# Kernel optimization log

Hardware: AMD Instinct MI355X
Metric: run time of the kernel (lower is better)

Reference implementation:

```python
import jax, jax.numpy as jnp
import numpy as np

B, S, D = 4, 2048, 1024
H = 16
HD = D // H


def setup_inputs() -> dict:
    key = jax.random.key(0)
    ks = jax.random.split(key, 5)
    scale = 0.02
    return {
        "x": jax.random.normal(ks[0], (B, S, D), dtype=jnp.float32),
        "wq": jax.random.normal(ks[1], (D, D), dtype=jnp.float32) * scale,
        "wk": jax.random.normal(ks[2], (D, D), dtype=jnp.float32) * scale,
        "wv": jax.random.normal(ks[3], (D, D), dtype=jnp.float32) * scale,
        "wo": jax.random.normal(ks[4], (D, D), dtype=jnp.float32) * scale,
    }


def reference(x, wq, wk, wv, wo):
    b, s, _ = x.shape
    # project and split heads: [b, h, s, hd]
    def proj(w):
        return jnp.einsum('bsd,de->bse', x, w).reshape(b, s, H, HD).transpose(0, 2, 1, 3)
    q, k, v = proj(wq), proj(wk), proj(wv)
    scores = jnp.einsum('bhqd,bhkd->bhqk', q, k)
    causal = jnp.tril(jnp.ones((s, s), dtype=bool))  # True = keep
    scores = jnp.where(causal, scores, -jnp.inf)
    attn = jax.nn.softmax(scores / jnp.sqrt(jnp.float32(HD)), axis=-1)
    ctx = jnp.einsum('bhqk,bhkd->bhqd', attn, v)
    ctx = ctx.transpose(0, 2, 1, 3).reshape(b, s, D)
    return jnp.einsum('bsd,de->bse', ctx, wo)
```

## Files before the change

kernel.cpp:

```cpp
#include <hip/hip_runtime.h>

#define S_LEN 2048
#define D_DIM 1024
#define NH    16
#define HD    64
#define BATCH 4
#define M_ROWS 8192

typedef __attribute__((ext_vector_type(8))) short bf16x8;
typedef __attribute__((ext_vector_type(4))) float f32x4;
typedef __attribute__((ext_vector_type(8))) unsigned short u16x8;

__device__ __forceinline__ unsigned short f2bf(float f) {
    unsigned u = __builtin_bit_cast(unsigned, f);
    u = (u + 0x7fffu + ((u >> 16) & 1u)) >> 16;
    return (unsigned short)u;
}
__device__ __forceinline__ unsigned pack2(float a, float b) {
    unsigned ua = __builtin_bit_cast(unsigned, a);
    unsigned ub = __builtin_bit_cast(unsigned, b);
    return ((ua + 0x8000u) >> 16) | ((ub + 0x8000u) & 0xffff0000u);
}

__device__ __forceinline__ void gload16(const void* g, void* l) {
    __builtin_amdgcn_global_load_lds((const __attribute__((address_space(1))) unsigned*)g,
                                     (__attribute__((address_space(3))) unsigned*)l,
                                     16, 0, 0);
}

__global__ __launch_bounds__(256) void castx_k(const float* __restrict__ x,
                                               unsigned short* __restrict__ o) {
    size_t i = (size_t)blockIdx.x * 256 + threadIdx.x;
    const float4* xf = (const float4*)x;
    float4 a = xf[2 * i], b = xf[2 * i + 1];
    u16x8 v;
    v[0] = f2bf(a.x); v[1] = f2bf(a.y); v[2] = f2bf(a.z); v[3] = f2bf(a.w);
    v[4] = f2bf(b.x); v[5] = f2bf(b.y); v[6] = f2bf(b.z); v[7] = f2bf(b.w);
    *(u16x8*)(o + i * 8) = v;
}

__global__ __launch_bounds__(256) void wprep_k(const float* __restrict__ w0, const float* __restrict__ w1,
                                               const float* __restrict__ w2, const float* __restrict__ w3,
                                               unsigned short* __restrict__ o0, unsigned short* __restrict__ o1,
                                               unsigned short* __restrict__ o2, unsigned short* __restrict__ o3) {
    __shared__ float sT[64][65];
    const float* w; unsigned short* o;
    switch (blockIdx.z) {
        case 0: w = w0; o = o0; break;
        case 1: w = w1; o = o1; break;
        case 2: w = w2; o = o2; break;
        default: w = w3; o = o3; break;
    }
    const float sc = (blockIdx.z == 0) ? 0.18033688011112042f : 1.0f;
    const int t = threadIdx.x;
    const int k0 = blockIdx.y * 64, n0 = blockIdx.x * 64;
    const int r = t >> 4, cq = t & 15;
#pragma unroll
    for (int it = 0; it < 4; ++it) {
        int k = r + it * 16;
        float4 v = *(const float4*)&w[(size_t)(k0 + k) * D_DIM + n0 + cq * 4];
        sT[k][cq * 4 + 0] = v.x; sT[k][cq * 4 + 1] = v.y;
        sT[k][cq * 4 + 2] = v.z; sT[k][cq * 4 + 3] = v.w;
    }
    __syncthreads();
    const int n = t >> 2, ch = t & 3;
    union { unsigned short s[8]; uint4 v; } p0, p1;
#pragma unroll
    for (int j = 0; j < 8; ++j) p0.s[j] = f2bf(sT[ch * 16 + j][n] * sc);
#pragma unroll
    for (int j = 0; j < 8; ++j) p1.s[j] = f2bf(sT[ch * 16 + 8 + j][n] * sc);
    *(uint4*)&o[(size_t)(n0 + n) * D_DIM + k0 + ch * 16]     = p0.v;
    *(uint4*)&o[(size_t)(n0 + n) * D_DIM + k0 + ch * 16 + 8] = p1.v;
}

__device__ __forceinline__ void gemm_core(const unsigned short* __restrict__ A,
                                          const unsigned short* __restrict__ Bt,
                                          unsigned short* sA, unsigned short* sB,
                                          int m0, int n0, int t, f32x4 acc[4][4])
{
    const int lane = t & 63, w = t >> 6;
    const int mm = lane & 15, quad = lane >> 4;
    const int wm = w >> 1, wn = w & 1;

    auto stage = [&](int k0, int bufi) {
#pragma unroll
        for (int it = 0; it < 2; ++it) {
            int idx = t + it * 256;
            int m = idx >> 2, j = idx & 3;
            int g = (j - (m >> 1)) & 3;
            gload16(A  + ((size_t)(m0 + m) * D_DIM + k0 + g * 8), (void*)&sA[bufi * 4096 + idx * 8]);
            gload16(Bt + ((size_t)(n0 + m) * D_DIM + k0 + g * 8), (void*)&sB[bufi * 4096 + idx * 8]);
        }
    };

    stage(0, 0);
    for (int kt = 0; kt < D_DIM / 32; ++kt) {
        const int bufo = (kt & 1) * 4096;
        __syncthreads();
        if (kt + 1 < D_DIM / 32) stage((kt + 1) * 32, 1 - (kt & 1));

        bf16x8 af[4], bfr[4];
#pragma unroll
        for (int mi = 0; mi < 4; ++mi) {
            int m = wm * 64 + mi * 16 + mm;
            int slot = (quad + (m >> 1)) & 3;
            af[mi] = *(const bf16x8*)&sA[bufo + m * 32 + slot * 8];
        }
#pragma unroll
        for (int ni = 0; ni < 4; ++ni) {
            int n = wn * 64 + ni * 16 + mm;
            int slot = (quad + (n >> 1)) & 3;
            bfr[ni] = *(const bf16x8*)&sB[bufo + n * 32 + slot * 8];
        }
#pragma unroll
        for (int mi = 0; mi < 4; ++mi)
#pragma unroll
            for (int ni = 0; ni < 4; ++ni)
                acc[mi][ni] = __builtin_amdgcn_mfma_f32_16x16x32_bf16(af[mi], bfr[ni], acc[mi][ni], 0, 0, 0);
    }
}

__global__ __launch_bounds__(256) void gemmqkv_k(const unsigned short* __restrict__ A,
                                                 const unsigned short* __restrict__ Bt,
                                                 unsigned short* __restrict__ qb,
                                                 unsigned short* __restrict__ kb,
                                                 unsigned short* __restrict__ vt)
{
    __shared__ unsigned short sA[2 * 128 * 32];
    __shared__ unsigned short sB[2 * 128 * 32];
    const int t = threadIdx.x;
    const int lane = t & 63, w = t >> 6;
    const int mm = lane & 15, quad = lane >> 4;
    const int wm = w >> 1, wn = w & 1;
    const int m0 = blockIdx.y * 128, n0 = blockIdx.x * 128;

    f32x4 acc[4][4];
#pragma unroll
    for (int i = 0; i < 4; ++i)
#pragma unroll
        for (int j = 0; j < 4; ++j) acc[i][j] = (f32x4){0.f, 0.f, 0.f, 0.f};

    gemm_core(A, Bt, sA, sB, m0, n0, t, acc);

    const int widx = n0 >> 10;
    if (widx == 2) {
#pragma unroll
        for (int mi = 0; mi < 4; ++mi) {
            int rglob = m0 + wm * 64 + mi * 16 + quad * 4;
            int bb = rglob >> 11, ss = rglob & (S_LEN - 1);
#pragma unroll
            for (int ni = 0; ni < 4; ++ni) {
                int c = (n0 & 1023) + wn * 64 + ni * 16 + mm;
                int h = c >> 6, hd = c & 63;
                union { unsigned short s[4]; unsigned long long ll; } pk;
#pragma unroll
                for (int r = 0; r < 4; ++r) pk.s[r] = f2bf(acc[mi][ni][r]);
                *(unsigned long long*)&vt[((size_t)(bb * NH + h) * HD + hd) * S_LEN + ss] = pk.ll;
            }
        }
    } else {
        unsigned short* outp = widx ? kb : qb;
        const int nl0 = n0 & 1023;
#pragma unroll
        for (int mi = 0; mi < 4; ++mi)
#pragma unroll
            for (int ni = 0; ni < 4; ++ni)
#pragma unroll
                for (int r = 0; r < 4; ++r)
                    outp[(size_t)(m0 + wm * 64 + mi * 16 + quad * 4 + r) * D_DIM +
                         nl0 + wn * 64 + ni * 16 + mm] = f2bf(acc[mi][ni][r]);
    }
}

__global__ __launch_bounds__(256) void gemmo_k(const unsigned short* __restrict__ A,
                                               const unsigned short* __restrict__ Bt,
                                               float* __restrict__ C)
{
    __shared__ unsigned short sA[2 * 128 * 32];
    __shared__ unsigned short sB[2 * 128 * 32];
    const int t = threadIdx.x;
    const int lane = t & 63, w = t >> 6;
    const int mm = lane & 15, quad = lane >> 4;
    const int wm = w >> 1, wn = w & 1;
    const int m0 = blockIdx.y * 128, n0 = blockIdx.x * 128;

    f32x4 acc[4][4];
#pragma unroll
    for (int i = 0; i < 4; ++i)
#pragma unroll
        for (int j = 0; j < 4; ++j) acc[i][j] = (f32x4){0.f, 0.f, 0.f, 0.f};

    gemm_core(A, Bt, sA, sB, m0, n0, t, acc);

#pragma unroll
    for (int mi = 0; mi < 4; ++mi)
#pragma unroll
        for (int ni = 0; ni < 4; ++ni)
#pragma unroll
            for (int r = 0; r < 4; ++r)
                C[(size_t)(m0 + wm * 64 + mi * 16 + quad * 4 + r) * D_DIM +
                  n0 + wn * 64 + ni * 16 + mm] = acc[mi][ni][r];
}

__global__ __launch_bounds__(512, 4) void attn_k(const unsigned short* __restrict__ Q,
                                                 const unsigned short* __restrict__ K,
                                                 const unsigned short* __restrict__ Vt,
                                                 unsigned short* __restrict__ ctx)
{
    __shared__ unsigned short sK [2][128 * 64];
    __shared__ unsigned short sVT[2][64 * 128];
    __shared__ unsigned short sP [128 * 64];
    const int t = threadIdx.x;
    const int lane = t & 63, w = t >> 6;
    const int mm = lane & 15, quad = lane >> 4;
    const int pair = blockIdx.x, bh = blockIdx.y;
    const int b = bh >> 4, hh = bh & 15;
    const size_t rowbase = (size_t)b * S_LEN;
    const int coff = hh * HD;
    const unsigned short* Vh = Vt + (size_t)bh * HD * S_LEN;

    auto stage = [&](int kt, int bufi) {
#pragma unroll
        for (int it = 0; it < 2; ++it) {
            int idx = t + it * 512;
            int key = idx >> 3, jk = idx & 7, gk = jk ^ (key & 7);
            gload16(K + (rowbase + kt * 128 + key) * D_DIM + coff + gk * 8,
                    (void*)&sK[bufi][idx * 8]);
            int hd = idx >> 4, jv = idx & 15, gv = jv ^ (hd & 15);
            gload16(Vh + (size_t)hd * S_LEN + kt * 128 + gv * 8,
                    (void*)&sVT[bufi][idx * 8]);
        }
    };

    u16x8 onesu;
#pragma unroll
    for (int j = 0; j < 8; ++j) onesu[j] = 0x3F80;
    const bf16x8 ones = __builtin_bit_cast(bf16x8, onesu);

    for (int sidx = 0; sidx < 2; ++sidx) {
        const int qt = sidx ? (15 - pair) : pair;
        const int q0 = qt * 128;

        bf16x8 qf[2];
#pragma unroll
        for (int kk = 0; kk < 2; ++kk)
            qf[kk] = *(const bf16x8*)(Q + (rowbase + q0 + w * 16 + mm) * D_DIM
                                        + coff + kk * 32 + quad * 8);
        f32x4 o[4], lacc;
        lacc = (f32x4){0.f, 0.f, 0.f, 0.f};
#pragma unroll
        for (int hf = 0; hf < 4; ++hf) o[hf] = (f32x4){0.f, 0.f, 0.f, 0.f};

        const int nkt = qt + 1;
        const int qr = q0 + w * 16 + mm;
        const int qrmax = q0 + w * 16 + 15;
        const int m = w * 16 + mm;

        stage(0, 0);
        for (int kt = 0; kt < nkt; ++kt) {
            const int buf = kt & 1;
            __syncthreads();
            if (kt + 1 < nkt) stage(kt + 1, 1 - buf);

#pragma unroll
            for (int kh = 0; kh < 2; ++kh) {
                const int k0 = kt * 128 + kh * 64;
                if (k0 > qrmax) continue;

                f32x4 sacc[4];
#pragma unroll
                for (int kf = 0; kf < 4; ++kf) sacc[kf] = (f32x4){0.f, 0.f, 0.f, 0.f};
#pragma unroll
                for (int kk = 0; kk < 2; ++kk) {
                    bf16x8 ak[4];
#pragma unroll
                    for (int kf = 0; kf < 4; ++kf) {
                        int key = kh * 64 + kf * 16 + mm;
                        int slot = (kk * 4 + quad) ^ (key & 7);
                        ak[kf] = *(const bf16x8*)&sK[buf][key * 64 + slot * 8];
                    }
#pragma unroll
                    for (int kf = 0; kf < 4; ++kf)
                        sacc[kf] = __builtin_amdgcn_mfma_f32_16x16x32_bf16(ak[kf], qf[kk], sacc[kf], 0, 0, 0);
                }

                const bool needmask = (k0 + 63) > (q0 + w * 16);
#pragma unroll
                for (int kf = 0; kf < 4; ++kf) {
                    float p[4];
#pragma unroll
                    for (int r = 0; r < 4; ++r) {
                        p[r] = __builtin_amdgcn_exp2f(sacc[kf][r]);
                        if (needmask && (k0 + kf * 16 + quad * 4 + r) > qr) p[r] = 0.f;
                    }
                    unsigned lo = pack2(p[0], p[1]), hi = pack2(p[2], p[3]);
                    int slot = (kf * 2 + (quad >> 1)) ^ (m & 7);
                    *(unsigned long long*)&sP[m * 64 + slot * 8 + (quad & 1) * 4] =
                        ((unsigned long long)hi << 32) | lo;
                }

#pragma unroll
                for (int kk = 0; kk < 2; ++kk) {
                    bf16x8 pf, vf[4];
                    {
                        int slot = (kk * 4 + quad) ^ (m & 7);
                        pf = *(const bf16x8*)&sP[m * 64 + slot * 8];
                    }
#pragma unroll
                    for (int hf = 0; hf < 4; ++hf) {
                        int hd = hf * 16 + mm;
                        int c = kh * 8 + kk * 4 + quad;
                        int slot = c ^ (hd & 15);
                        vf[hf] = *(const bf16x8*)&sVT[buf][hd * 128 + slot * 8];
                    }
                    lacc = __builtin_amdgcn_mfma_f32_16x16x32_bf16(pf, ones, lacc, 0, 0, 0);
#pragma unroll
                    for (int hf = 0; hf < 4; ++hf)
                        o[hf] = __builtin_amdgcn_mfma_f32_16x16x32_bf16(pf, vf[hf], o[hf], 0, 0, 0);
                }
            }
        }
        __syncthreads();

#pragma unroll
        for (int r = 0; r < 4; ++r) {
            float inv = 1.f / lacc[r];
            int row = q0 + w * 16 + quad * 4 + r;
#pragma unroll
            for (int hf = 0; hf < 4; ++hf)
                ctx[(rowbase + row) * D_DIM + coff + hf * 16 + mm] = f2bf(o[hf][r] * inv);
        }
    }
}

extern "C" void kernel_launch(void* const* d_in, const int* in_sizes, int n_in,
                              void* d_out, int out_size, void* d_ws, size_t ws_size,
                              hipStream_t stream)
{
    const float* x  = (const float*)d_in[0];
    const float* wq = (const float*)d_in[1];
    const float* wk = (const float*)d_in[2];
    const float* wv = (const float*)d_in[3];
    const float* wo = (const float*)d_in[4];

    const size_t XE = (size_t)M_ROWS * D_DIM;
    const size_t WE = (size_t)D_DIM * D_DIM;
    unsigned short* ws  = (unsigned short*)d_ws;
    unsigned short* xbf = ws;
    unsigned short* wt0 = xbf + XE;
    unsigned short* wt1 = wt0 + WE;
    unsigned short* wt2 = wt1 + WE;
    unsigned short* wt3 = wt2 + WE;
    unsigned short* qb  = wt3 + WE;
    unsigned short* kb  = qb + XE;
    unsigned short* vt  = kb + XE;
    unsigned short* cb  = vt + XE;

    castx_k<<<dim3(M_ROWS * D_DIM / (256 * 8)), 256, 0, stream>>>(x, xbf);
    wprep_k<<<dim3(16, 16, 4), 256, 0, stream>>>(wq, wk, wv, wo, wt0, wt1, wt2, wt3);

    gemmqkv_k<<<dim3(3 * D_DIM / 128, M_ROWS / 128), 256, 0, stream>>>(xbf, wt0, qb, kb, vt);

    attn_k<<<dim3(8, BATCH * NH), 512, 0, stream>>>(qb, kb, vt, cb);

    gemmo_k<<<dim3(D_DIM / 128, M_ROWS / 128), 256, 0, stream>>>(cb, wt3, (float*)d_out);
}
```

Before: 280.2 us.

## Single-buffer GEMM staging and shrink attention key tiles to 64

The GEMM core drops double-buffered LDS staging for a single buffer, loading and then synchronizing before each k-step. This halves GEMM shared memory but stops overlapping loads with MFMA work. The attention kernel moves from 128-key to 64-key tiles with a matching swizzle, halving its LDS footprint and masking less work per tile, at the cost of twice as many iterations and barriers.

```diff
diff --git a/kernel.cpp b/kernel.cpp
--- a/kernel.cpp
+++ b/kernel.cpp
@@ -82,35 +82,30 @@
     const int mm = lane & 15, quad = lane >> 4;
     const int wm = w >> 1, wn = w & 1;
 
-    auto stage = [&](int k0, int bufi) {
+    for (int k0 = 0; k0 < D_DIM; k0 += 32) {
+        __syncthreads();
 #pragma unroll
         for (int it = 0; it < 2; ++it) {
             int idx = t + it * 256;
             int m = idx >> 2, j = idx & 3;
             int g = (j - (m >> 1)) & 3;
-            gload16(A  + ((size_t)(m0 + m) * D_DIM + k0 + g * 8), (void*)&sA[bufi * 4096 + idx * 8]);
-            gload16(Bt + ((size_t)(n0 + m) * D_DIM + k0 + g * 8), (void*)&sB[bufi * 4096 + idx * 8]);
-        }
-    };
-
-    stage(0, 0);
-    for (int kt = 0; kt < D_DIM / 32; ++kt) {
-        const int bufo = (kt & 1) * 4096;
+            gload16(A  + ((size_t)(m0 + m) * D_DIM + k0 + g * 8), (void*)&sA[idx * 8]);
+            gload16(Bt + ((size_t)(n0 + m) * D_DIM + k0 + g * 8), (void*)&sB[idx * 8]);
+        }
         __syncthreads();
-        if (kt + 1 < D_DIM / 32) stage((kt + 1) * 32, 1 - (kt & 1));
 
         bf16x8 af[4], bfr[4];
 #pragma unroll
         for (int mi = 0; mi < 4; ++mi) {
             int m = wm * 64 + mi * 16 + mm;
             int slot = (quad + (m >> 1)) & 3;
-            af[mi] = *(const bf16x8*)&sA[bufo + m * 32 + slot * 8];
+            af[mi] = *(const bf16x8*)&sA[m * 32 + slot * 8];
         }
 #pragma unroll
         for (int ni = 0; ni < 4; ++ni) {
             int n = wn * 64 + ni * 16 + mm;
             int slot = (quad + (n >> 1)) & 3;
-            bfr[ni] = *(const bf16x8*)&sB[bufo + n * 32 + slot * 8];
+            bfr[ni] = *(const bf16x8*)&sB[n * 32 + slot * 8];
         }
 #pragma unroll
         for (int mi = 0; mi < 4; ++mi)
@@ -126,8 +121,8 @@
                                                  unsigned short* __restrict__ kb,
                                                  unsigned short* __restrict__ vt)
 {
-    __shared__ unsigned short sA[2 * 128 * 32];
-    __shared__ unsigned short sB[2 * 128 * 32];
+    __shared__ unsigned short sA[128 * 32];
+    __shared__ unsigned short sB[128 * 32];
     const int t = threadIdx.x;
     const int lane = t & 63, w = t >> 6;
     const int mm = lane & 15, quad = lane >> 4;
@@ -176,8 +171,8 @@
                                                const unsigned short* __restrict__ Bt,
                                                float* __restrict__ C)
 {
-    __shared__ unsigned short sA[2 * 128 * 32];
-    __shared__ unsigned short sB[2 * 128 * 32];
+    __shared__ unsigned short sA[128 * 32];
+    __shared__ unsigned short sB[128 * 32];
     const int t = threadIdx.x;
     const int lane = t & 63, w = t >> 6;
     const int mm = lane & 15, quad = lane >> 4;
@@ -207,8 +202,8 @@
                                                  const unsigned short* __restrict__ Vt,
                                                  unsigned short* __restrict__ ctx)
 {
-    __shared__ unsigned short sK [2][128 * 64];
-    __shared__ unsigned short sVT[2][64 * 128];
+    __shared__ unsigned short sK [2][64 * 64];
+    __shared__ unsigned short sVT[2][64 * 64];
     __shared__ unsigned short sP [128 * 64];
     const int t = threadIdx.x;
     const int lane = t & 63, w = t >> 6;
@@ -219,18 +214,8 @@
     const int coff = hh * HD;
     const unsigned short* Vh = Vt + (size_t)bh * HD * S_LEN;
 
-    auto stage = [&](int kt, int bufi) {
-#pragma unroll
-        for (int it = 0; it < 2; ++it) {
-            int idx = t + it * 512;
-            int key = idx >> 3, jk = idx & 7, gk = jk ^ (key & 7);
-            gload16(K + (rowbase + kt * 128 + key) * D_DIM + coff + gk * 8,
-                    (void*)&sK[bufi][idx * 8]);
-            int hd = idx >> 4, jv = idx & 15, gv = jv ^ (hd & 15);
-            gload16(Vh + (size_t)hd * S_LEN + kt * 128 + gv * 8,
-                    (void*)&sVT[bufi][idx * 8]);
-        }
-    };
+    const int sc_ = t >> 3, sj = t & 7;
+    const int sgk = sj ^ (sc_ & 7);
 
     u16x8 onesu;
 #pragma unroll
@@ -251,73 +236,76 @@
 #pragma unroll
         for (int hf = 0; hf < 4; ++hf) o[hf] = (f32x4){0.f, 0.f, 0.f, 0.f};
 
-        const int nkt = qt + 1;
+        const int nkt = 2 * qt + 2;
         const int qr = q0 + w * 16 + mm;
         const int qrmax = q0 + w * 16 + 15;
         const int m = w * 16 + mm;
 
-        stage(0, 0);
+        gload16(K  + (rowbase + sc_) * D_DIM + coff + sgk * 8, (void*)&sK[0][t * 8]);
+        gload16(Vh + (size_t)sc_ * S_LEN + sgk * 8,            (void*)&sVT[0][t * 8]);
+
         for (int kt = 0; kt < nkt; ++kt) {
             const int buf = kt & 1;
             __syncthreads();
-            if (kt + 1 < nkt) stage(kt + 1, 1 - buf);
-
-#pragma unroll
-            for (int kh = 0; kh < 2; ++kh) {
-                const int k0 = kt * 128 + kh * 64;
-                if (k0 > qrmax) continue;
-
-                f32x4 sacc[4];
-#pragma unroll
-                for (int kf = 0; kf < 4; ++kf) sacc[kf] = (f32x4){0.f, 0.f, 0.f, 0.f};
-#pragma unroll
-                for (int kk = 0; kk < 2; ++kk) {
-                    bf16x8 ak[4];
-#pragma unroll
-                    for (int kf = 0; kf < 4; ++kf) {
-                        int key = kh * 64 + kf * 16 + mm;
-                        int slot = (kk * 4 + quad) ^ (key & 7);
-                        ak[kf] = *(const bf16x8*)&sK[buf][key * 64 + slot * 8];
-                    }
-#pragma unroll
-                    for (int kf = 0; kf < 4; ++kf)
-                        sacc[kf] = __builtin_amdgcn_mfma_f32_16x16x32_bf16(ak[kf], qf[kk], sacc[kf], 0, 0, 0);
+            if (kt + 1 < nkt) {
+                const int k1 = (kt + 1) * 64;
+                gload16(K  + (rowbase + k1 + sc_) * D_DIM + coff + sgk * 8,
+                        (void*)&sK[1 - buf][t * 8]);
+                gload16(Vh + (size_t)sc_ * S_LEN + k1 + sgk * 8,
+                        (void*)&sVT[1 - buf][t * 8]);
+            }
+            const int k0 = kt * 64;
+            if (k0 > qrmax) continue;
+
+            f32x4 sacc[4];
+#pragma unroll
+            for (int kf = 0; kf < 4; ++kf) sacc[kf] = (f32x4){0.f, 0.f, 0.f, 0.f};
+#pragma unroll
+            for (int kk = 0; kk < 2; ++kk) {
+                bf16x8 ak[4];
+#pragma unroll
+                for (int kf = 0; kf < 4; ++kf) {
+                    int key = kf * 16 + mm;
+                    int slot = (kk * 4 + quad) ^ (key & 7);
+                    ak[kf] = *(const bf16x8*)&sK[buf][key * 64 + slot * 8];
                 }
-
-                const bool needmask = (k0 + 63) > (q0 + w * 16);
-#pragma unroll
-                for (int kf = 0; kf < 4; ++kf) {
-                    float p[4];
-#pragma unroll
-                    for (int r = 0; r < 4; ++r) {
-                        p[r] = __builtin_amdgcn_exp2f(sacc[kf][r]);
-                        if (needmask && (k0 + kf * 16 + quad * 4 + r) > qr) p[r] = 0.f;
-                    }
-                    unsigned lo = pack2(p[0], p[1]), hi = pack2(p[2], p[3]);
-                    int slot = (kf * 2 + (quad >> 1)) ^ (m & 7);
-                    *(unsigned long long*)&sP[m * 64 + slot * 8 + (quad & 1) * 4] =
-                        ((unsigned long long)hi << 32) | lo;
+#pragma unroll
+                for (int kf = 0; kf < 4; ++kf)
+                    sacc[kf] = __builtin_amdgcn_mfma_f32_16x16x32_bf16(ak[kf], qf[kk], sacc[kf], 0, 0, 0);
+            }
+
+            const bool needmask = (k0 + 63) > (q0 + w * 16);
+#pragma unroll
+            for (int kf = 0; kf < 4; ++kf) {
+                float p[4];
+#pragma unroll
+                for (int r = 0; r < 4; ++r) {
+                    p[r] = __builtin_amdgcn_exp2f(sacc[kf][r]);
+                    if (needmask && (k0 + kf * 16 + quad * 4 + r) > qr) p[r] = 0.f;
                 }
-
-#pragma unroll
-                for (int kk = 0; kk < 2; ++kk) {
-                    bf16x8 pf, vf[4];
-                    {
-                        int slot = (kk * 4 + quad) ^ (m & 7);
-                        pf = *(const bf16x8*)&sP[m * 64 + slot * 8];
-                    }
-#pragma unroll
-                    for (int hf = 0; hf < 4; ++hf) {
-                        int hd = hf * 16 + mm;
-                        int c = kh * 8 + kk * 4 + quad;
-                        int slot = c ^ (hd & 15);
-                        vf[hf] = *(const bf16x8*)&sVT[buf][hd * 128 + slot * 8];
-                    }
-                    lacc = __builtin_amdgcn_mfma_f32_16x16x32_bf16(pf, ones, lacc, 0, 0, 0);
-#pragma unroll
-                    for (int hf = 0; hf < 4; ++hf)
-                        o[hf] = __builtin_amdgcn_mfma_f32_16x16x32_bf16(pf, vf[hf], o[hf], 0, 0, 0);
+                unsigned lo = pack2(p[0], p[1]), hi = pack2(p[2], p[3]);
+                int slot = (kf * 2 + (quad >> 1)) ^ (m & 7);
+                *(unsigned long long*)&sP[m * 64 + slot * 8 + (quad & 1) * 4] =
+                    ((unsigned long long)hi << 32) | lo;
+            }
+
+#pragma unroll
+            for (int kk = 0; kk < 2; ++kk) {
+                bf16x8 pf, vf[4];
+                {
+                    int slot = (kk * 4 + quad) ^ (m & 7);
+                    pf = *(const bf16x8*)&sP[m * 64 + slot * 8];
                 }
+#pragma unroll
+                for (int hf = 0; hf < 4; ++hf) {
+                    int hd = hf * 16 + mm;
+                    int slot = (kk * 4 + quad) ^ (hd & 7);
+                    vf[hf] = *(const bf16x8*)&sVT[buf][hd * 64 + slot * 8];
+                }
+                lacc = __builtin_amdgcn_mfma_f32_16x16x32_bf16(pf, ones, lacc, 0, 0, 0);
+#pragma unroll
+                for (int hf = 0; hf < 4; ++hf)
+                    o[hf] = __builtin_amdgcn_mfma_f32_16x16x32_bf16(pf, vf[hf], o[hf], 0, 0, 0);
             }
         }
         __syncthreads();
```

After: 261.7 us. 6.6% less time.
